# Kernel tuning notes

Hardware: AMD Instinct MI355X
Metric: run time of the kernel (lower is better)

## Reference

```python
import jax, jax.numpy as jnp
import numpy as np

SCALE = 32.0  # hardcoded self.scale in the module


def fwht(x):
    """Fast Walsh-Hadamard transform along last dim (power-of-2 length).
    Equivalent to x @ H_n (Sylvester Hadamard), unnormalized."""
    orig_shape = x.shape
    n = orig_shape[-1]
    x = x.reshape(-1, n)
    h = 2
    while h <= n:
        x = x.reshape(-1, n // h, h)
        half = h // 2
        a = x[:, :, :half]
        b = x[:, :, half:]
        x = jnp.concatenate([a + b, a - b], axis=-1)
        h *= 2
    return x.reshape(orig_shape)


def setup_inputs() -> dict:
    key = jax.random.key(0)
    k1, k2, k3, k4, k5 = jax.random.split(key, 5)
    B, S, N, M = 8, 2048, 4096, 4096
    x = jax.random.normal(k1, (B, S, N), dtype=jnp.float32)
    W = jax.random.normal(k2, (M, N), dtype=jnp.float32) * 0.02  # nn.Linear weight [out, in]
    SU = jax.random.uniform(k3, (N,), dtype=jnp.float32, minval=0.5, maxval=1.5)
    SV = jax.random.uniform(k4, (M,), dtype=jnp.float32, minval=0.5, maxval=1.5)
    Wscale = jax.random.uniform(k5, (M,), dtype=jnp.float32, minval=0.5, maxval=1.5)
    return {"x": x, "W": W, "SU": SU, "SV": SV, "Wscale": Wscale}


def reference(x, W, SU, SV, Wscale):
    n = SU.shape[0]
    m = SV.shape[0]
    inv_sqrt_n = 1.0 / np.sqrt(n).astype(np.float32)
    inv_sqrt_m = 1.0 / np.sqrt(m).astype(np.float32)
    h = x.reshape(-1, n) * SU                       # per-channel input scale
    h = fwht(h) * (inv_sqrt_n / SCALE)              # normalized Hadamard rotation / scale
    h = jnp.einsum('tn,mn->tm', h, W) * Wscale      # linear + per-channel weight scale
    h = fwht(h) * inv_sqrt_m                        # inverse (normalized) Hadamard rotation
    h = h * (SV * SCALE)                            # per-channel output scale * scale
    return h.reshape(*x.shape[:-1], m)
```

## Files before the change

kernel.cpp:

```cpp
#include <hip/hip_runtime.h>
#include <hip/hip_bf16.h>

typedef __bf16 bf16x8 __attribute__((ext_vector_type(8)));
typedef float f32x4 __attribute__((ext_vector_type(4)));

__device__ __forceinline__ void gload16(const void* g, void* l) {
  __builtin_amdgcn_global_load_lds(
      (const __attribute__((address_space(1))) void*)g,
      (__attribute__((address_space(3))) void*)l, 16, 0, 0);
}

__device__ __forceinline__ unsigned short f2bf(float f) {
  __hip_bfloat16 h = __float2bfloat16(f);
  union { __hip_bfloat16 h; unsigned short u; } c;
  c.h = h;
  return c.u;
}

__device__ __forceinline__ void fwht16(float v[16]) {
#pragma unroll
  for (int s = 1; s < 16; s <<= 1) {
#pragma unroll
    for (int i = 0; i < 16; i++) {
      if ((i & s) == 0) {
        float a = v[i], b = v[i | s];
        v[i] = a + b;
        v[i | s] = a - b;
      }
    }
  }
}

__global__ __launch_bounds__(256) void fwht1_kernel(
    const float* __restrict__ x, const float* __restrict__ SU,
    unsigned short* __restrict__ H1) {
  __shared__ float lds[256 * 17];
  const int t = threadIdx.x;
  const size_t row = blockIdx.x;
  const float* xr = x + row * 4096;
  float v[16];
#pragma unroll
  for (int n2 = 0; n2 < 16; n2++) {
    int n = n2 * 256 + t;
    v[n2] = xr[n] * SU[n];
  }
  fwht16(v);
  const int n1 = t >> 4, n0 = t & 15;
#pragma unroll
  for (int j2 = 0; j2 < 16; j2++) lds[(j2 * 16 + n1) * 17 + n0] = v[j2];
  __syncthreads();
#pragma unroll
  for (int k = 0; k < 16; k++) v[k] = lds[((t >> 4) * 16 + k) * 17 + (t & 15)];
  fwht16(v);
#pragma unroll
  for (int k = 0; k < 16; k++) lds[((t >> 4) * 16 + k) * 17 + (t & 15)] = v[k];
  __syncthreads();
#pragma unroll
  for (int k = 0; k < 16; k++) v[k] = lds[t * 17 + k];
  fwht16(v);
  const float cst = 1.0f / 2048.0f;
  union { unsigned short u[16]; uint4 q[2]; } o;
#pragma unroll
  for (int k = 0; k < 16; k++) o.u[k] = f2bf(v[k] * cst);
  uint4* dst = (uint4*)(H1 + row * 4096 + (size_t)t * 16);
  dst[0] = o.q[0];
  dst[1] = o.q[1];
}

__global__ __launch_bounds__(256) void convw_kernel(
    const float4* __restrict__ W4, const float* __restrict__ Wscale,
    uint2* __restrict__ Wb4, int total4, int Nq) {
  int i = blockIdx.x * 256 + threadIdx.x;
  if (i >= total4) return;
  float4 w = W4[i];
  float s = Wscale[i / Nq];
  unsigned int lo = (unsigned)f2bf(w.x * s) | ((unsigned)f2bf(w.y * s) << 16);
  unsigned int hi = (unsigned)f2bf(w.z * s) | ((unsigned)f2bf(w.w * s) << 16);
  Wb4[i] = make_uint2(lo, hi);
}


#define BARRIER()                          \
  do {                                     \
    asm volatile("" ::: "memory");         \
    __builtin_amdgcn_s_barrier();          \
    asm volatile("" ::: "memory");         \
  } while (0)
#define GATE4() asm volatile("s_waitcnt vmcnt(4)" ::: "memory")
#define GATE0() asm volatile("s_waitcnt vmcnt(0)" ::: "memory")

__device__ __forceinline__ void stage_half(const unsigned short* __restrict__ g,
                                           unsigned short* l, int tid, int K) {
#pragma unroll
  for (int i = 0; i < 2; i++) {
    int idx = i * 512 + tid;
    int r = idx >> 3;
    int c = (idx & 7) ^ (r & 7);
    gload16(g + (size_t)r * K + c * 8, l + idx * 8);
  }
}

#define STAGE_A(d, hh, kt) \
  stage_half(Abase + (size_t)(hh) * 128 * K + (size_t)(kt) * 64, &As[d][(hh) * 8192], tid, K)
#define STAGE_B(d, hh, kt) \
  stage_half(Bbase + (size_t)(hh) * 128 * K + (size_t)(kt) * 64, &Bs[d][(hh) * 8192], tid, K)

#define LOAD_A(d, h)                                                          \
  {                                                                           \
    _Pragma("unroll") for (int i = 0; i < 4; i++) {                           \
      _Pragma("unroll") for (int ks = 0; ks < 2; ks++) {                      \
        int r = wm * 128 + (h) * 64 + i * 16 + fr;                            \
        int kc = ks * 4 + lhi;                                                \
        ah[i][ks] = *(const bf16x8*)&As[d][r * 64 + ((kc ^ (r & 7)) << 3)];   \
      }                                                                       \
    }                                                                         \
  }

#define LOAD_B(d, v, dst)                                                     \
  {                                                                           \
    _Pragma("unroll") for (int j = 0; j < 2; j++) {                           \
      _Pragma("unroll") for (int ks = 0; ks < 2; ks++) {                      \
        int r = wn * 64 + (v) * 32 + j * 16 + fr;                             \
        int kc = ks * 4 + lhi;                                                \
        dst[j][ks] = *(const bf16x8*)&Bs[d][r * 64 + ((kc ^ (r & 7)) << 3)];  \
      }                                                                       \
    }                                                                         \
  }

#define MFMA_PH(h, v, bvx)                                                    \
  {                                                                           \
    __builtin_amdgcn_s_setprio(1);                                            \
    _Pragma("unroll") for (int i = 0; i < 4; i++)                             \
      _Pragma("unroll") for (int j = 0; j < 2; j++)                           \
        _Pragma("unroll") for (int ks = 0; ks < 2; ks++)                      \
          acc[(h)*4 + i][(v)*2 + j] = __builtin_amdgcn_mfma_f32_16x16x32_bf16( \
              ah[i][ks], bvx[j][ks], acc[(h)*4 + i][(v)*2 + j], 0, 0, 0);     \
    __builtin_amdgcn_s_setprio(0);                                            \
  }

__global__ __launch_bounds__(512, 2) void gemm8_kernel(
    const unsigned short* __restrict__ A, const unsigned short* __restrict__ B,
    float* __restrict__ C, int M, int K, int NT) {
  __shared__ __align__(16) unsigned short As[2][256 * 64];
  __shared__ __align__(16) unsigned short Bs[2][256 * 64];
  const int nbn = M >> 8;
  const int cpx = gridDim.x >> 3;
  int bid = blockIdx.x;
  bid = (bid & 7) * cpx + (bid >> 3);
  const int brow = (bid / nbn) << 8;
  const int bcol = (bid % nbn) << 8;
  const int tid = threadIdx.x;
  const int lane = tid & 63;
  const int w = tid >> 6;
  const int wm = w >> 2;
  const int wn = w & 3;
  const int fr = lane & 15;
  const int lhi = lane >> 4;

  const unsigned short* Abase = A + (size_t)brow * K;
  const unsigned short* Bbase = B + (size_t)bcol * K;

  f32x4 acc[8][4];
#pragma unroll
  for (int i = 0; i < 8; i++)
#pragma unroll
    for (int j = 0; j < 4; j++) acc[i][j] = (f32x4){0.f, 0.f, 0.f, 0.f};
  bf16x8 ah[4][2], bv0[2][2], bv1[2][2];

  STAGE_B(0, 0, 0);
  STAGE_B(0, 1, 0);
  STAGE_A(0, 0, 0);
  STAGE_A(0, 1, 0);
  STAGE_B(1, 0, 1);
  STAGE_B(1, 1, 1);
  GATE4();
  BARRIER();

  for (int t = 0; t < NT / 2; ++t) {
    const bool last = (t == NT / 2 - 1);
    const int k1 = 2 * t + 1, k2 = 2 * t + 2, k3 = 2 * t + 3;
    LOAD_A(0, 0);
    LOAD_B(0, 0, bv0);
    STAGE_A(1, 0, k1);
    BARRIER();
    MFMA_PH(0, 0, bv0);
    BARRIER();
    LOAD_B(0, 1, bv1);
    STAGE_A(1, 1, k1);
    BARRIER();
    MFMA_PH(0, 1, bv1);
    BARRIER();
    LOAD_A(0, 1);
    if (!last) STAGE_B(0, 0, k2);
    BARRIER();
    MFMA_PH(1, 1, bv1);
    BARRIER();
    if (!last) STAGE_B(0, 1, k2);
    BARRIER();
    MFMA_PH(1, 0, bv0);
    if (!last) { GATE4(); } else { GATE0(); }
    BARRIER();
    LOAD_A(1, 0);
    LOAD_B(1, 0, bv0);
    if (!last) STAGE_A(0, 0, k2);
    BARRIER();
    MFMA_PH(0, 0, bv0);
    BARRIER();
    LOAD_B(1, 1, bv1);
    if (!last) STAGE_A(0, 1, k2);
    BARRIER();
    MFMA_PH(0, 1, bv1);
    BARRIER();
    LOAD_A(1, 1);
    if (!last) STAGE_B(1, 0, k3);
    BARRIER();
    MFMA_PH(1, 1, bv1);
    BARRIER();
    if (!last) STAGE_B(1, 1, k3);
    BARRIER();
    MFMA_PH(1, 0, bv0);
    if (!last) GATE4();
    BARRIER();
  }

  const int crow0 = brow + wm * 128 + lhi * 4;
  const int ccol0 = bcol + wn * 64 + fr;
#pragma unroll
  for (int mi = 0; mi < 8; mi++)
#pragma unroll
    for (int nj = 0; nj < 4; nj++)
#pragma unroll
      for (int q = 0; q < 4; q++)
        C[(size_t)(crow0 + mi * 16 + q) * M + ccol0 + nj * 16] = acc[mi][nj][q];
}

__global__ __launch_bounds__(256) void fwht2_kernel(
    float* __restrict__ Y, const float* __restrict__ SV) {
  __shared__ float lds[256 * 17];
  const int t = threadIdx.x;
  const size_t row = blockIdx.x;
  float* yr = Y + row * 4096;
  float v[16];
#pragma unroll
  for (int n2 = 0; n2 < 16; n2++) v[n2] = yr[n2 * 256 + t];
  fwht16(v);
  const int n1 = t >> 4, n0 = t & 15;
#pragma unroll
  for (int j2 = 0; j2 < 16; j2++) lds[(j2 * 16 + n1) * 17 + n0] = v[j2];
  __syncthreads();
#pragma unroll
  for (int k = 0; k < 16; k++) v[k] = lds[((t >> 4) * 16 + k) * 17 + (t & 15)];
  fwht16(v);
#pragma unroll
  for (int k = 0; k < 16; k++) lds[((t >> 4) * 16 + k) * 17 + (t & 15)] = v[k];
  __syncthreads();
#pragma unroll
  for (int k = 0; k < 16; k++) v[k] = lds[t * 17 + k];
  fwht16(v);
  float outv[16];
#pragma unroll
  for (int k = 0; k < 16; k++) outv[k] = v[k] * 0.5f * SV[(size_t)t * 16 + k];
  float4* dst = (float4*)(yr + (size_t)t * 16);
#pragma unroll
  for (int k = 0; k < 4; k++)
    dst[k] = make_float4(outv[4 * k], outv[4 * k + 1], outv[4 * k + 2],
                         outv[4 * k + 3]);
}

extern "C" void kernel_launch(void* const* d_in, const int* in_sizes, int n_in,
                              void* d_out, int out_size, void* d_ws,
                              size_t ws_size, hipStream_t stream) {
  const float* x = (const float*)d_in[0];
  const float* W = (const float*)d_in[1];
  const float* SU = (const float*)d_in[2];
  const float* SV = (const float*)d_in[3];
  const float* Wscale = (const float*)d_in[4];
  const int N = in_sizes[2];
  const int M = in_sizes[3];
  const int T = in_sizes[0] / N;

  unsigned short* H1 = (unsigned short*)d_ws;
  unsigned short* Wb = H1 + (size_t)T * N;
  float* out = (float*)d_out;

  fwht1_kernel<<<T, 256, 0, stream>>>(x, SU, H1);
  const int total4 = (int)(((long)M * N) / 4);
  convw_kernel<<<(total4 + 255) / 256, 256, 0, stream>>>(
      (const float4*)W, Wscale, (uint2*)Wb, total4, N / 4);
  const int NT = N / 64;
  gemm8_kernel<<<(T / 256) * (M / 256), 512, 0, stream>>>(H1, Wb, out, M, N, NT);
  fwht2_kernel<<<T, 256, 0, stream>>>(out, SV);
}
```

Measured before the change: 758.4 us.

## Restructure GEMM LDS pipeline with quarter-tile A staging and early B prefetch

Reorders the double-buffered GEMM main loop so A and B for the next k-tile are staged together in the prologue. A staging is split into quarter tiles interleaved with the MFMA phases. The B fragment for the next phase is loaded from LDS before the preceding MFMA phase, and one barrier pair per half-iteration is removed. The aim is to spread global-to-LDS traffic more evenly and hide LDS read latency behind matrix ops. In exchange it uses extra registers for a second B fragment buffer and relies on delicate vmcnt gating that could race if the counts are wrong.

Result: no change. 761.8 us (+0.5%).

```diff
diff --git a/kernel.cpp b/kernel.cpp
--- a/kernel.cpp
+++ b/kernel.cpp
@@ -87,6 +87,7 @@
     asm volatile("" ::: "memory");         \
   } while (0)
 #define GATE4() asm volatile("s_waitcnt vmcnt(4)" ::: "memory")
+#define GATE8() asm volatile("s_waitcnt vmcnt(8)" ::: "memory")
 #define GATE0() asm volatile("s_waitcnt vmcnt(0)" ::: "memory")
 
 __device__ __forceinline__ void stage_half(const unsigned short* __restrict__ g,
@@ -99,11 +100,19 @@
     gload16(g + (size_t)r * K + c * 8, l + idx * 8);
   }
 }
+__device__ __forceinline__ void stage_quarter(
+    const unsigned short* __restrict__ g, unsigned short* l, int tid, int K) {
+  int r = tid >> 3;
+  int c = (tid & 7) ^ (r & 7);
+  gload16(g + (size_t)r * K + c * 8, l + tid * 8);
+}
 
 #define STAGE_A(d, hh, kt) \
   stage_half(Abase + (size_t)(hh) * 128 * K + (size_t)(kt) * 64, &As[d][(hh) * 8192], tid, K)
 #define STAGE_B(d, hh, kt) \
   stage_half(Bbase + (size_t)(hh) * 128 * K + (size_t)(kt) * 64, &Bs[d][(hh) * 8192], tid, K)
+#define STAGE_AQ(d, q, kt) \
+  stage_quarter(Abase + (size_t)(q) * 64 * K + (size_t)(kt) * 64, &As[d][(q) * 4096], tid, K)
 
 #define LOAD_A(d, h)                                                          \
   {                                                                           \
@@ -165,61 +174,68 @@
   for (int i = 0; i < 8; i++)
 #pragma unroll
     for (int j = 0; j < 4; j++) acc[i][j] = (f32x4){0.f, 0.f, 0.f, 0.f};
-  bf16x8 ah[4][2], bv0[2][2], bv1[2][2];
-
+  bf16x8 ah[4][2], bvA[2][2], bvB[2][2], bv1[2][2];
+
+  STAGE_A(0, 0, 0);
+  STAGE_A(0, 1, 0);
   STAGE_B(0, 0, 0);
   STAGE_B(0, 1, 0);
-  STAGE_A(0, 0, 0);
-  STAGE_A(0, 1, 0);
+  STAGE_A(1, 0, 1);
+  STAGE_A(1, 1, 1);
   STAGE_B(1, 0, 1);
   STAGE_B(1, 1, 1);
-  GATE4();
+  GATE8();
   BARRIER();
-
-  for (int t = 0; t < NT / 2; ++t) {
-    const bool last = (t == NT / 2 - 1);
-    const int k1 = 2 * t + 1, k2 = 2 * t + 2, k3 = 2 * t + 3;
+  LOAD_B(0, 0, bvA);
+
+  const int NTT = NT / 2;
+#pragma unroll 1
+  for (int t = 0; t < NTT; ++t) {
+    const bool last = (t == NTT - 1);
+    const int u2 = 2 * t + 2, u3 = 2 * t + 3;
     LOAD_A(0, 0);
-    LOAD_B(0, 0, bv0);
-    STAGE_A(1, 0, k1);
-    BARRIER();
-    MFMA_PH(0, 0, bv0);
+    BARRIER();
+    MFMA_PH(0, 0, bvA);
     BARRIER();
     LOAD_B(0, 1, bv1);
-    STAGE_A(1, 1, k1);
+    if (!last) { STAGE_AQ(0, 0, u2); STAGE_AQ(0, 2, u2); }
     BARRIER();
     MFMA_PH(0, 1, bv1);
     BARRIER();
     LOAD_A(0, 1);
-    if (!last) STAGE_B(0, 0, k2);
+    if (!last) STAGE_B(0, 0, u2);
     BARRIER();
     MFMA_PH(1, 1, bv1);
     BARRIER();
-    if (!last) STAGE_B(0, 1, k2);
-    BARRIER();
-    MFMA_PH(1, 0, bv0);
     if (!last) { GATE4(); } else { GATE0(); }
+    LOAD_B(1, 0, bvB);
+    if (!last) { STAGE_B(0, 1, u2); STAGE_AQ(0, 1, u2); STAGE_AQ(0, 3, u2); }
+    BARRIER();
+    MFMA_PH(1, 0, bvA);
     BARRIER();
     LOAD_A(1, 0);
-    LOAD_B(1, 0, bv0);
-    if (!last) STAGE_A(0, 0, k2);
-    BARRIER();
-    MFMA_PH(0, 0, bv0);
+    BARRIER();
+    MFMA_PH(0, 0, bvB);
     BARRIER();
     LOAD_B(1, 1, bv1);
-    if (!last) STAGE_A(0, 1, k2);
+    if (!last) { STAGE_AQ(1, 0, u3); STAGE_AQ(1, 2, u3); }
     BARRIER();
     MFMA_PH(0, 1, bv1);
     BARRIER();
     LOAD_A(1, 1);
-    if (!last) STAGE_B(1, 0, k3);
+    if (!last) STAGE_B(1, 0, u3);
     BARRIER();
     MFMA_PH(1, 1, bv1);
     BARRIER();
-    if (!last) STAGE_B(1, 1, k3);
-    BARRIER();
-    MFMA_PH(1, 0, bv0);
-    if (!last) GATE4();
+    if (!last) {
+      GATE4();
+      LOAD_B(0, 0, bvA);
+      STAGE_B(1, 1, u3);
+      STAGE_AQ(1, 1, u3);
+      STAGE_AQ(1, 3, u3);
+    }
+    BARRIER();
+    MFMA_PH(1, 0, bvB);
     BARRIER();
   }
 
```

## Restructure GEMM main loop staging schedule with fewer barriers and tighter vmcnt gates

Applied to the files above, without the earlier changes.

Reorders the double-buffered LDS staging in the bf16 GEMM main loop so that each half-tile global→LDS load is issued right after the barrier that frees its buffer. This removes about half of the workgroup barriers per iteration and changes the wait gate from vmcnt(4) to vmcnt(2). The aim is to cut barrier stalls and keep memory loads overlapped with MFMA work. The trade-off is that less prefetch is in flight when each gate is reached, and the correctness of buffer reuse now depends on the exact order of the new schedule.

Result: slower. 806.8 us (+6.4%).

```diff
diff --git a/kernel.cpp b/kernel.cpp
--- a/kernel.cpp
+++ b/kernel.cpp
@@ -86,7 +86,7 @@
     __builtin_amdgcn_s_barrier();          \
     asm volatile("" ::: "memory");         \
   } while (0)
-#define GATE4() asm volatile("s_waitcnt vmcnt(4)" ::: "memory")
+#define GATE2() asm volatile("s_waitcnt vmcnt(2)" ::: "memory")
 #define GATE0() asm volatile("s_waitcnt vmcnt(0)" ::: "memory")
 
 __device__ __forceinline__ void stage_half(const unsigned short* __restrict__ g,
@@ -101,15 +101,15 @@
 }
 
 #define STAGE_A(d, hh, kt) \
-  stage_half(Abase + (size_t)(hh) * 128 * K + (size_t)(kt) * 64, &As[d][(hh) * 8192], tid, K)
+  stage_half(Abase + (size_t)(hh)*128 * K + (size_t)(kt)*64, &As[d][(hh)*8192], tid, K)
 #define STAGE_B(d, hh, kt) \
-  stage_half(Bbase + (size_t)(hh) * 128 * K + (size_t)(kt) * 64, &Bs[d][(hh) * 8192], tid, K)
+  stage_half(Bbase + (size_t)(hh)*128 * K + (size_t)(kt)*64, &Bs[d][(hh)*8192], tid, K)
 
 #define LOAD_A(d, h)                                                          \
   {                                                                           \
     _Pragma("unroll") for (int i = 0; i < 4; i++) {                           \
       _Pragma("unroll") for (int ks = 0; ks < 2; ks++) {                      \
-        int r = wm * 128 + (h) * 64 + i * 16 + fr;                            \
+        int r = wm * 128 + (h)*64 + i * 16 + fr;                              \
         int kc = ks * 4 + lhi;                                                \
         ah[i][ks] = *(const bf16x8*)&As[d][r * 64 + ((kc ^ (r & 7)) << 3)];   \
       }                                                                       \
@@ -120,7 +120,7 @@
   {                                                                           \
     _Pragma("unroll") for (int j = 0; j < 2; j++) {                           \
       _Pragma("unroll") for (int ks = 0; ks < 2; ks++) {                      \
-        int r = wn * 64 + (v) * 32 + j * 16 + fr;                             \
+        int r = wn * 64 + (v)*32 + j * 16 + fr;                               \
         int kc = ks * 4 + lhi;                                                \
         dst[j][ks] = *(const bf16x8*)&Bs[d][r * 64 + ((kc ^ (r & 7)) << 3)];  \
       }                                                                       \
@@ -167,60 +167,51 @@
     for (int j = 0; j < 4; j++) acc[i][j] = (f32x4){0.f, 0.f, 0.f, 0.f};
   bf16x8 ah[4][2], bv0[2][2], bv1[2][2];
 
+  STAGE_A(0, 0, 0);
+  STAGE_A(0, 1, 0);
   STAGE_B(0, 0, 0);
   STAGE_B(0, 1, 0);
-  STAGE_A(0, 0, 0);
-  STAGE_A(0, 1, 0);
-  STAGE_B(1, 0, 1);
-  STAGE_B(1, 1, 1);
-  GATE4();
-  BARRIER();
-
-  for (int t = 0; t < NT / 2; ++t) {
-    const bool last = (t == NT / 2 - 1);
-    const int k1 = 2 * t + 1, k2 = 2 * t + 2, k3 = 2 * t + 3;
+  STAGE_A(1, 0, 1);
+
+  const int NTT = NT / 2;
+#pragma unroll 1
+  for (int t = 0; t < NTT; ++t) {
+    const bool last = (t == NTT - 1);
+    const int u1 = 2 * t + 1, u2 = 2 * t + 2, u3 = 2 * t + 3;
+    GATE2();
+    BARRIER();
+    STAGE_A(1, 1, u1);
     LOAD_A(0, 0);
     LOAD_B(0, 0, bv0);
-    STAGE_A(1, 0, k1);
-    BARRIER();
     MFMA_PH(0, 0, bv0);
     BARRIER();
+    STAGE_B(1, 0, u1);
     LOAD_B(0, 1, bv1);
-    STAGE_A(1, 1, k1);
-    BARRIER();
     MFMA_PH(0, 1, bv1);
     BARRIER();
+    STAGE_B(1, 1, u1);
     LOAD_A(0, 1);
-    if (!last) STAGE_B(0, 0, k2);
-    BARRIER();
     MFMA_PH(1, 1, bv1);
     BARRIER();
-    if (!last) STAGE_B(0, 1, k2);
-    BARRIER();
+    if (!last) STAGE_A(0, 0, u2);
     MFMA_PH(1, 0, bv0);
-    if (!last) { GATE4(); } else { GATE0(); }
-    BARRIER();
+    if (last) { GATE0(); } else { GATE2(); }
+    BARRIER();
+    if (!last) STAGE_A(0, 1, u2);
     LOAD_A(1, 0);
     LOAD_B(1, 0, bv0);
-    if (!last) STAGE_A(0, 0, k2);
-    BARRIER();
     MFMA_PH(0, 0, bv0);
     BARRIER();
+    if (!last) STAGE_B(0, 0, u2);
     LOAD_B(1, 1, bv1);
-    if (!last) STAGE_A(0, 1, k2);
-    BARRIER();
     MFMA_PH(0, 1, bv1);
     BARRIER();
+    if (!last) STAGE_B(0, 1, u2);
     LOAD_A(1, 1);
-    if (!last) STAGE_B(1, 0, k3);
-    BARRIER();
     MFMA_PH(1, 1, bv1);
     BARRIER();
-    if (!last) STAGE_B(1, 1, k3);
-    BARRIER();
+    if (!last) STAGE_A(1, 0, u3);
     MFMA_PH(1, 0, bv0);
-    if (!last) GATE4();
-    BARRIER();
   }
 
   const int crow0 = brow + wm * 128 + lhi * 4;
```
